# Kernel tuning notes

Measured on AMD Instinct MI355X. Metric: run time of the kernel, lower is better.

The kernel has to match this reference:

```python
import jax, jax.numpy as jnp
import numpy as np

VOCAB, EMBED, HIDDEN, PAD = 32000, 512, 1024, 3

def setup_inputs() -> dict:
    key = jax.random.key(0)
    ks = jax.random.split(key, 7)
    B, S = 16, 256
    input_ids = jax.random.randint(ks[0], (B, S), 0, VOCAB)
    hidden = jnp.zeros((B, HIDDEN), dtype=jnp.float32)
    sc = 0.02
    emb_table = jax.random.normal(ks[1], (VOCAB, EMBED), jnp.float32) * sc
    Wxh_w = jax.random.normal(ks[2], (HIDDEN, EMBED), jnp.float32) * sc
    Wxh_b = jax.random.normal(ks[3], (HIDDEN,), jnp.float32) * sc
    Whh_w = jax.random.normal(ks[4], (HIDDEN, HIDDEN), jnp.float32) * sc
    Who_w = jax.random.normal(ks[5], (VOCAB, HIDDEN), jnp.float32) * sc
    Who_b = jax.random.normal(ks[6], (VOCAB,), jnp.float32) * sc
    return {"input_ids": input_ids, "hidden": hidden, "emb_table": emb_table,
            "Wxh_w": Wxh_w, "Wxh_b": Wxh_b, "Whh_w": Whh_w,
            "Who_w": Who_w, "Who_b": Who_b}

def reference(input_ids, hidden, emb_table, Wxh_w, Wxh_b, Whh_w, Who_w, Who_b):
    # padding_idx: row PAD of the embedding is zero
    pad_mask = (jnp.arange(VOCAB) != PAD).astype(emb_table.dtype)
    table = emb_table * pad_mask[:, None]
    embeds = table[input_ids]                      # [B, S, E]
    # precompute input projection for all steps: [B, S, H]
    xproj = jnp.einsum('bse,he->bsh', embeds, Wxh_w) + Wxh_b

    def step(h, xp_t):                             # xp_t: [B, H]
        h_new = jnp.tanh(xp_t + h @ Whh_w.T)
        return h_new, h_new

    h_final, h_all = jax.lax.scan(step, hidden, jnp.swapaxes(xproj, 0, 1))
    # h_all: [S, B, H] -> logits [B, S, V]
    logits = jnp.einsum('sbh,vh->bsv', h_all, Who_w) + Who_b
    return (logits, h_final)
```

## Files before the change

### kernel.cpp

```cpp
#include <hip/hip_runtime.h>
#include <stdint.h>

#define NB 16
#define NS 256
#define NV 32000
#define NE 512
#define NH 1024
#define PAD_IDX 3

#define WS_XP    0L
#define WS_HCH   16777216L
#define WS_WHO   25198592L
#define WS_FLG   90734592L
#define WS_NEED  90800384L

typedef __attribute__((ext_vector_type(8))) short bf16x8;
typedef __attribute__((ext_vector_type(4))) float f32x4;
typedef __attribute__((ext_vector_type(4))) uint32_t u32x4;

__device__ __forceinline__ uint16_t f2bf(float f){
  union { float f; uint32_t u; } v; v.f = f;
  return (uint16_t)((v.u + 0x7fffu + ((v.u >> 16) & 1u)) >> 16);
}

__device__ __forceinline__ bf16x8 pack8(float4 a, float4 b){
  bf16x8 r;
  r[0]=(short)f2bf(a.x); r[1]=(short)f2bf(a.y); r[2]=(short)f2bf(a.z); r[3]=(short)f2bf(a.w);
  r[4]=(short)f2bf(b.x); r[5]=(short)f2bf(b.y); r[6]=(short)f2bf(b.z); r[7]=(short)f2bf(b.w);
  return r;
}

__device__ __forceinline__ u32x4 load_coh16(const void* p){
  u32x4 r;
  asm volatile("global_load_dwordx4 %0, %1, off sc0 sc1" : "=v"(r) : "v"(p) : "memory");
  return r;
}
__device__ __forceinline__ uint32_t load_coh4(const void* p){
  uint32_t r;
  asm volatile("global_load_dword %0, %1, off sc0 sc1" : "=v"(r) : "v"(p) : "memory");
  return r;
}
__device__ __forceinline__ void store_coh8(void* p, uint64_t v){
  asm volatile("global_store_dwordx2 %0, %1, off sc0 sc1" :: "v"(p), "v"(v) : "memory");
}
__device__ __forceinline__ void store_coh4(void* p, uint32_t v){
  asm volatile("global_store_dword %0, %1, off sc0 sc1" :: "v"(p), "v"(v) : "memory");
}
__device__ __forceinline__ void store_nt4(void* p, float v){
  asm volatile("global_store_dword %0, %1, off nt" :: "v"(p), "v"(v) : "memory");
}

__device__ __forceinline__ u32x4 umax4(u32x4 a, u32x4 b){
  u32x4 r;
  r[0] = a[0] > b[0] ? a[0] : b[0];
  r[1] = a[1] > b[1] ? a[1] : b[1];
  r[2] = a[2] > b[2] ? a[2] : b[2];
  r[3] = a[3] > b[3] ? a[3] : b[3];
  return r;
}

__device__ __forceinline__ float tanh_fast(float x){
  x = fminf(fmaxf(x, -10.f), 10.f);
  float t = __builtin_amdgcn_exp2f(x * 2.885390081777927f);
  return (t - 1.0f) * __builtin_amdgcn_rcpf(t + 1.0f);
}

__global__ void k_init(const float* __restrict__ hidden, uint16_t* __restrict__ hch,
                       uint32_t* __restrict__ flg){
  long idx = (long)blockIdx.x * 256 + threadIdx.x;
  ((u32x4*)(hch + (long)NB * NH))[idx] = (u32x4){~0u, ~0u, ~0u, ~0u};
  if (idx < NB * NH) hch[idx] = f2bf(hidden[idx]);
  if (idx < 512) flg[idx] = 0u;
}

__global__ void k_cvt(const float* __restrict__ src, uint32_t* __restrict__ dst){
  long idx = (long)blockIdx.x * 256 + threadIdx.x;
  const float4* p = (const float4*)src;
  float4 a = p[idx*2], b = p[idx*2+1];
  u32x4 d;
  d[0] = (uint32_t)f2bf(a.x) | ((uint32_t)f2bf(a.y) << 16);
  d[1] = (uint32_t)f2bf(a.z) | ((uint32_t)f2bf(a.w) << 16);
  d[2] = (uint32_t)f2bf(b.x) | ((uint32_t)f2bf(b.y) << 16);
  d[3] = (uint32_t)f2bf(b.z) | ((uint32_t)f2bf(b.w) << 16);
  ((u32x4*)dst)[idx] = d;
}

__global__ __launch_bounds__(256) void k_xproj(
    const int* __restrict__ ids, const float* __restrict__ tab,
    const float* __restrict__ wxh, const float* __restrict__ bxh,
    float* __restrict__ xp){
  int bid = blockIdx.x;
  int tm = bid & 63, tn = bid >> 6;
  int Mb = tm * 64, Nb = tn * 64;
  int tid = threadIdx.x;
  int w = tid >> 6, l = tid & 63;
  int lr = l & 15, lk = l >> 4;

  int m = Mb + w*16 + lr;
  int id = ids[m];
  const float* arow = tab + (long)id * NE;
  bool pad = (id == PAD_IDX);

  f32x4 acc[4];
  #pragma unroll
  for (int j = 0; j < 4; ++j) acc[j] = (f32x4){0.f,0.f,0.f,0.f};

  for (int k0 = 0; k0 < NE; k0 += 32){
    int k = k0 + lk*8;
    bf16x8 af = (bf16x8){0,0,0,0,0,0,0,0};
    if (!pad){
      float4 a = *(const float4*)(arow + k);
      float4 b = *(const float4*)(arow + k + 4);
      af = pack8(a, b);
    }
    #pragma unroll
    for (int j = 0; j < 4; ++j){
      const float* brow = wxh + (long)(Nb + j*16 + lr) * NE + k;
      float4 x = *(const float4*)brow;
      float4 y = *(const float4*)(brow + 4);
      bf16x8 bf_ = pack8(x, y);
      acc[j] = __builtin_amdgcn_mfma_f32_16x16x32_bf16(af, bf_, acc[j], 0, 0, 0);
    }
  }
  #pragma unroll
  for (int j = 0; j < 4; ++j){
    int n = Nb + j*16 + lr;
    float bias = bxh[n];
    #pragma unroll
    for (int r = 0; r < 4; ++r){
      int row = Mb + w*16 + lk*4 + r;
      xp[(long)row * NH + n] = acc[j][r] + bias;
    }
  }
}

__global__ __launch_bounds__(256, 2) void k_fused(
    const float* __restrict__ whh, const float* __restrict__ xp,
    uint16_t* __restrict__ hch, const uint16_t* __restrict__ whobf,
    const float* __restrict__ whob, uint32_t* __restrict__ allvis,
    uint32_t* __restrict__ fin, float* __restrict__ out,
    float* __restrict__ hfin){
  __shared__ __align__(16) char smem[17*1024];
  const int bid = blockIdx.x;
  const int tid = threadIdx.x;

  if (bid < 64){
    f32x4*    accbuf = (f32x4*)smem;
    uint16_t* hs2    = (uint16_t*)(smem + 6144);
    const int wv = tid >> 6;
    const int l  = tid & 63;
    const int j0 = bid * 16;
    const int lr = l & 15, lk = l >> 4;
    __builtin_amdgcn_s_setprio(2);

    bf16x8 bfrag[8];
    #pragma unroll
    for (int kk = 0; kk < 8; ++kk){
      const float* s0 = whh + (long)(j0 + lr) * NH + (wv*8 + kk)*32 + lk*8;
      float4 a = *(const float4*)s0;
      float4 b = *(const float4*)(s0 + 4);
      bfrag[kk] = pack8(a, b);
    }

    float xpreg[4];
    if (wv == 0){
      #pragma unroll
      for (int r = 0; r < 4; ++r)
        xpreg[r] = xp[((long)(lk*4 + r) * NS + 0) * NH + j0 + lr];
    }

    const char* hbase = (const char*)hch;
    for (int t = 0; t < NS; ++t){
      const char* hsrc = hbase + (long)t * NB * NH * 2 + lr * 2048 + wv * 512 + lk * 16;
      u32x4 hfrag[8];
      while (true){
        #pragma unroll
        for (int kk = 0; kk < 8; ++kk)
          hfrag[kk] = load_coh16(hsrc + kk * 64);
        asm volatile("s_waitcnt vmcnt(0)" ::: "memory");
        __builtin_amdgcn_sched_barrier(0);
        u32x4 m4 = hfrag[0];
        #pragma unroll
        for (int kk = 1; kk < 8; ++kk) m4 = umax4(m4, hfrag[kk]);
        uint32_t m01 = m4[0] > m4[1] ? m4[0] : m4[1];
        uint32_t m23 = m4[2] > m4[3] ? m4[2] : m4[3];
        uint32_t m = m01 > m23 ? m01 : m23;
        if (__all(m != 0xFFFFFFFFu)) break;
      }
      __builtin_amdgcn_sched_barrier(0);

      f32x4 a0 = (f32x4){0.f,0.f,0.f,0.f}, a1 = a0;
      #pragma unroll
      for (int kk = 0; kk < 8; kk += 2){
        a0 = __builtin_amdgcn_mfma_f32_16x16x32_bf16(*(const bf16x8*)&hfrag[kk  ], bfrag[kk  ], a0, 0, 0, 0);
        a1 = __builtin_amdgcn_mfma_f32_16x16x32_bf16(*(const bf16x8*)&hfrag[kk+1], bfrag[kk+1], a1, 0, 0, 0);
      }
      f32x4 acc = a0 + a1;

      if (wv != 0)
        accbuf[((t & 1)*3 + (wv-1))*64 + l] = acc;
      __syncthreads();

      if (wv == 0){
        if (bid == 0 && l == 0) store_coh4(allvis + t, 1u);
        f32x4 o0 = accbuf[((t & 1)*3 + 0)*64 + l];
        f32x4 o1 = accbuf[((t & 1)*3 + 1)*64 + l];
        f32x4 o2 = accbuf[((t & 1)*3 + 2)*64 + l];
        f32x4 osum = (acc + o0) + (o1 + o2);
        uint16_t* hb = hs2 + (t & 1)*256;
        #pragma unroll
        for (int r = 0; r < 4; ++r){
          int b = lk*4 + r;
          float hv = tanh_fast(xpreg[r] + osum[r]);
          hb[b*16 + lr] = f2bf(hv);
          if (t == NS-1) hfin[b*NH + j0 + lr] = hv;
        }
        asm volatile("s_waitcnt lgkmcnt(0)" ::: "memory");
        __builtin_amdgcn_sched_barrier(0);
        int rb = l >> 2, cc = l & 3;
        uint32_t w0 = *(const uint32_t*)&hb[rb*16 + cc*4];
        uint32_t w1 = *(const uint32_t*)&hb[rb*16 + cc*4 + 2];
        char* dst = (char*)hch + (long)(t+1) * NB * NH * 2 + rb * 2048 + j0*2 + cc*8;
        store_coh8(dst, ((uint64_t)w1 << 32) | (uint64_t)w0);
        if (t + 1 < NS){
          #pragma unroll
          for (int r = 0; r < 4; ++r)
            xpreg[r] = xp[((long)(lk*4 + r) * NS + (t+1)) * NH + j0 + lr];
        }
      }
    }
    if (wv == 0){
      asm volatile("s_waitcnt vmcnt(0)" ::: "memory");
      if (l == 0) store_coh4(fin + bid, 1u);
    }
    return;
  }

  uint16_t* As = (uint16_t*)smem;
  uint16_t* Bs = (uint16_t*)(smem + 8192);
  int tile = bid - 64;
  int tm = tile / 250;
  int tn = tile % 250;
  int Mb = tm * 128, Nb = tn * 128;
  int hs = tm * 8 + 8;

  if (hs < 256){
    while (true){
      uint32_t f = load_coh4(allvis + hs);
      asm volatile("s_waitcnt vmcnt(0)" ::: "memory");
      __builtin_amdgcn_sched_barrier(0);
      if (__syncthreads_count(f == 0u) == 0) break;
      __builtin_amdgcn_s_sleep(16);
    }
  } else {
    const uint32_t* gp = fin + (tid & 63);
    while (true){
      uint32_t f = load_coh4(gp);
      asm volatile("s_waitcnt vmcnt(0)" ::: "memory");
      __builtin_amdgcn_sched_barrier(0);
      if (__syncthreads_count(f == 0u) == 0) break;
      __builtin_amdgcn_s_sleep(16);
    }
  }

  int wv = tid >> 6, l = tid & 63;
  int wm = wv >> 1, wn = wv & 1;
  int lr = l & 15, lk = l >> 4;

  int r0 = tid >> 2, c0 = tid & 3;
  int r1 = r0 + 64;
  const uint16_t* pa0 = hch + (long)(Mb + r0 + 16) * NH + c0*8;
  const uint16_t* pa1 = hch + (long)(Mb + r1 + 16) * NH + c0*8;
  const uint16_t* pb0 = whobf + (long)(Nb + r0) * NH + c0*8;
  const uint16_t* pb1 = whobf + (long)(Nb + r1) * NH + c0*8;
  int da0 = r0*4 + (c0 ^ (r0 & 3));
  int da1 = r1*4 + (c0 ^ (r1 & 3));

  u32x4 ra0 = *(const u32x4*)pa0;
  u32x4 ra1 = *(const u32x4*)pa1;
  u32x4 rb0 = *(const u32x4*)pb0;
  u32x4 rb1 = *(const u32x4*)pb1;

  f32x4 acc[4][4];
  #pragma unroll
  for (int i = 0; i < 4; ++i)
    #pragma unroll
    for (int jj = 0; jj < 4; ++jj) acc[i][jj] = (f32x4){0.f,0.f,0.f,0.f};

  for (int kt = 0; kt < 32; ++kt){
    ((u32x4*)As)[da0] = ra0;
    ((u32x4*)As)[da1] = ra1;
    ((u32x4*)Bs)[da0] = rb0;
    ((u32x4*)Bs)[da1] = rb1;
    __syncthreads();
    if (kt != 31){
      int off = (kt + 1) * 32;
      ra0 = *(const u32x4*)(pa0 + off);
      ra1 = *(const u32x4*)(pa1 + off);
      rb0 = *(const u32x4*)(pb0 + off);
      rb1 = *(const u32x4*)(pb1 + off);
    }
    bf16x8 af[4], bg_[4];
    #pragma unroll
    for (int i = 0; i < 4; ++i){
      int ra = wm*64 + i*16 + lr;
      int rb = wn*64 + i*16 + lr;
      af[i]  = *(const bf16x8*)&((const u32x4*)As)[ra*4 + (lk ^ (ra & 3))];
      bg_[i] = *(const bf16x8*)&((const u32x4*)Bs)[rb*4 + (lk ^ (rb & 3))];
    }
    #pragma unroll
    for (int i = 0; i < 4; ++i)
      #pragma unroll
      for (int jj = 0; jj < 4; ++jj)
        acc[i][jj] = __builtin_amdgcn_mfma_f32_16x16x32_bf16(af[i], bg_[jj], acc[i][jj], 0, 0, 0);
    __syncthreads();
  }

  #pragma unroll
  for (int jj = 0; jj < 4; ++jj){
    int col = Nb + wn*64 + jj*16 + lr;
    float bias = whob[col];
    #pragma unroll
    for (int i = 0; i < 4; ++i){
      #pragma unroll
      for (int rr = 0; rr < 4; ++rr){
        int m = Mb + wm*64 + i*16 + lk*4 + rr;
        long orow = (long)((m & 15) * 256 + (m >> 4));
        store_nt4(&out[orow * NV + col], acc[i][jj][rr] + bias);
      }
    }
  }
}

extern "C" void kernel_launch(void* const* d_in, const int* in_sizes, int n_in,
                              void* d_out, int out_size, void* d_ws, size_t ws_size,
                              hipStream_t stream){
  (void)in_sizes; (void)n_in; (void)out_size;
  if (ws_size < (size_t)WS_NEED) return;

  const int*   ids    = (const int*)  d_in[0];
  const float* hidden = (const float*)d_in[1];
  const float* table  = (const float*)d_in[2];
  const float* wxh    = (const float*)d_in[3];
  const float* bxh    = (const float*)d_in[4];
  const float* whh    = (const float*)d_in[5];
  const float* who    = (const float*)d_in[6];
  const float* whob   = (const float*)d_in[7];

  char* ws = (char*)d_ws;
  float*    xp     = (float*)   (ws + WS_XP);
  uint16_t* hchain = (uint16_t*)(ws + WS_HCH);
  uint16_t* whobf  = (uint16_t*)(ws + WS_WHO);
  uint32_t* allvis = (uint32_t*)(ws + WS_FLG);
  uint32_t* fin    = allvis + 260;
  float* out    = (float*)d_out;
  float* hfinal = out + (long)NB * NS * NV;

  k_init <<<2048,  256, 0, stream>>>(hidden, hchain, allvis);
  k_cvt  <<<16000, 256, 0, stream>>>(who, (uint32_t*)whobf);
  k_xproj<<<1024,  256, 0, stream>>>(ids, table, wxh, bxh, xp);
  k_fused<<<8064,  256, 0, stream>>>(whh, xp, hchain, whobf, whob,
                                     allvis, fin, out, hfinal);
}
```

Measured before the change: 1.126 ms.

## Shrink recurrence to 16 blocks with full-K per wave via LDS-staged h

New measurement: 1.002 ms. 1.12x faster.

```diff
diff --git a/kernel.cpp b/kernel.cpp
--- a/kernel.cpp
+++ b/kernel.cpp
@@ -140,105 +140,98 @@
     const float* __restrict__ whob, uint32_t* __restrict__ allvis,
     uint32_t* __restrict__ fin, float* __restrict__ out,
     float* __restrict__ hfin){
-  __shared__ __align__(16) char smem[17*1024];
+  __shared__ __align__(16) char smem[35*1024];
   const int bid = blockIdx.x;
   const int tid = threadIdx.x;
 
-  if (bid < 64){
-    f32x4*    accbuf = (f32x4*)smem;
-    uint16_t* hs2    = (uint16_t*)(smem + 6144);
-    const int wv = tid >> 6;
-    const int l  = tid & 63;
-    const int j0 = bid * 16;
+  if (bid < 16){
+    uint16_t* hlds = (uint16_t*)smem;
+    uint16_t* hs2  = (uint16_t*)(smem + 32768);
+    const int wv = tid >> 6, l = tid & 63;
     const int lr = l & 15, lk = l >> 4;
+    const int base = bid*64 + wv*16;
     __builtin_amdgcn_s_setprio(2);
 
-    bf16x8 bfrag[8];
-    #pragma unroll
-    for (int kk = 0; kk < 8; ++kk){
-      const float* s0 = whh + (long)(j0 + lr) * NH + (wv*8 + kk)*32 + lk*8;
-      float4 a = *(const float4*)s0;
-      float4 b = *(const float4*)(s0 + 4);
-      bfrag[kk] = pack8(a, b);
+    bf16x8 wf[32];
+    #pragma unroll
+    for (int kk = 0; kk < 32; ++kk){
+      const float* s0 = whh + (long)(base + lr) * NH + kk*32 + lk*8;
+      wf[kk] = pack8(*(const float4*)s0, *(const float4*)(s0 + 4));
     }
 
     float xpreg[4];
-    if (wv == 0){
-      #pragma unroll
-      for (int r = 0; r < 4; ++r)
-        xpreg[r] = xp[((long)(lk*4 + r) * NS + 0) * NH + j0 + lr];
-    }
-
-    const char* hbase = (const char*)hch;
+    #pragma unroll
+    for (int r = 0; r < 4; ++r)
+      xpreg[r] = xp[((long)(lk*4 + r) * NS + 0) * NH + base + lr];
+
     for (int t = 0; t < NS; ++t){
-      const char* hsrc = hbase + (long)t * NB * NH * 2 + lr * 2048 + wv * 512 + lk * 16;
-      u32x4 hfrag[8];
-      while (true){
+      {
+        const char* ps = (const char*)hch + ((long)t * NB + (l >> 2)) * 2048
+                       + wv*512 + (l & 3)*128;
+        u32x4 hf[8];
+        while (true){
+          #pragma unroll
+          for (int j = 0; j < 8; ++j) hf[j] = load_coh16(ps + j*16);
+          asm volatile("s_waitcnt vmcnt(0)" ::: "memory");
+          __builtin_amdgcn_sched_barrier(0);
+          u32x4 m4 = hf[0];
+          #pragma unroll
+          for (int j = 1; j < 8; ++j) m4 = umax4(m4, hf[j]);
+          uint32_t m01 = m4[0] > m4[1] ? m4[0] : m4[1];
+          uint32_t m23 = m4[2] > m4[3] ? m4[2] : m4[3];
+          uint32_t m = m01 > m23 ? m01 : m23;
+          if (__all(m != 0xFFFFFFFFu)) break;
+        }
+        __builtin_amdgcn_sched_barrier(0);
+        int batch = l >> 2;
         #pragma unroll
-        for (int kk = 0; kk < 8; ++kk)
-          hfrag[kk] = load_coh16(hsrc + kk * 64);
-        asm volatile("s_waitcnt vmcnt(0)" ::: "memory");
-        __builtin_amdgcn_sched_barrier(0);
-        u32x4 m4 = hfrag[0];
-        #pragma unroll
-        for (int kk = 1; kk < 8; ++kk) m4 = umax4(m4, hfrag[kk]);
-        uint32_t m01 = m4[0] > m4[1] ? m4[0] : m4[1];
-        uint32_t m23 = m4[2] > m4[3] ? m4[2] : m4[3];
-        uint32_t m = m01 > m23 ? m01 : m23;
-        if (__all(m != 0xFFFFFFFFu)) break;
-      }
-      __builtin_amdgcn_sched_barrier(0);
+        for (int j = 0; j < 8; ++j){
+          int cib = wv*32 + (l & 3)*8 + j;
+          ((u32x4*)hlds)[batch*128 + (cib ^ (batch & 7))] = hf[j];
+        }
+      }
+      __syncthreads();
+      if (bid == 0 && tid == 0) store_coh4(allvis + t, 1u);
 
       f32x4 a0 = (f32x4){0.f,0.f,0.f,0.f}, a1 = a0;
       #pragma unroll
-      for (int kk = 0; kk < 8; kk += 2){
-        a0 = __builtin_amdgcn_mfma_f32_16x16x32_bf16(*(const bf16x8*)&hfrag[kk  ], bfrag[kk  ], a0, 0, 0, 0);
-        a1 = __builtin_amdgcn_mfma_f32_16x16x32_bf16(*(const bf16x8*)&hfrag[kk+1], bfrag[kk+1], a1, 0, 0, 0);
+      for (int kk = 0; kk < 32; kk += 2){
+        bf16x8 af0 = *(const bf16x8*)&((const u32x4*)hlds)[lr*128 + (( kk   *4 + lk) ^ (lr & 7))];
+        bf16x8 af1 = *(const bf16x8*)&((const u32x4*)hlds)[lr*128 + (((kk+1)*4 + lk) ^ (lr & 7))];
+        a0 = __builtin_amdgcn_mfma_f32_16x16x32_bf16(af0, wf[kk  ], a0, 0, 0, 0);
+        a1 = __builtin_amdgcn_mfma_f32_16x16x32_bf16(af1, wf[kk+1], a1, 0, 0, 0);
       }
       f32x4 acc = a0 + a1;
 
-      if (wv != 0)
-        accbuf[((t & 1)*3 + (wv-1))*64 + l] = acc;
+      #pragma unroll
+      for (int r = 0; r < 4; ++r){
+        float hv = tanh_fast(xpreg[r] + acc[r]);
+        hs2[(lk*4 + r)*64 + wv*16 + lr] = f2bf(hv);
+        if (t == NS-1) hfin[(long)(lk*4 + r) * NH + base + lr] = hv;
+      }
       __syncthreads();
 
-      if (wv == 0){
-        if (bid == 0 && l == 0) store_coh4(allvis + t, 1u);
-        f32x4 o0 = accbuf[((t & 1)*3 + 0)*64 + l];
-        f32x4 o1 = accbuf[((t & 1)*3 + 1)*64 + l];
-        f32x4 o2 = accbuf[((t & 1)*3 + 2)*64 + l];
-        f32x4 osum = (acc + o0) + (o1 + o2);
-        uint16_t* hb = hs2 + (t & 1)*256;
+      {
+        int row = tid >> 4, ch = tid & 15;
+        uint64_t v = *(const uint64_t*)&hs2[row*64 + ch*4];
+        char* dst = (char*)hch + ((long)(t+1) * NB + row) * 2048 + (bid*64 + ch*4)*2;
+        store_coh8(dst, v);
+      }
+      if (t + 1 < NS){
         #pragma unroll
-        for (int r = 0; r < 4; ++r){
-          int b = lk*4 + r;
-          float hv = tanh_fast(xpreg[r] + osum[r]);
-          hb[b*16 + lr] = f2bf(hv);
-          if (t == NS-1) hfin[b*NH + j0 + lr] = hv;
-        }
-        asm volatile("s_waitcnt lgkmcnt(0)" ::: "memory");
-        __builtin_amdgcn_sched_barrier(0);
-        int rb = l >> 2, cc = l & 3;
-        uint32_t w0 = *(const uint32_t*)&hb[rb*16 + cc*4];
-        uint32_t w1 = *(const uint32_t*)&hb[rb*16 + cc*4 + 2];
-        char* dst = (char*)hch + (long)(t+1) * NB * NH * 2 + rb * 2048 + j0*2 + cc*8;
-        store_coh8(dst, ((uint64_t)w1 << 32) | (uint64_t)w0);
-        if (t + 1 < NS){
-          #pragma unroll
-          for (int r = 0; r < 4; ++r)
-            xpreg[r] = xp[((long)(lk*4 + r) * NS + (t+1)) * NH + j0 + lr];
-        }
-      }
-    }
-    if (wv == 0){
-      asm volatile("s_waitcnt vmcnt(0)" ::: "memory");
-      if (l == 0) store_coh4(fin + bid, 1u);
-    }
+        for (int r = 0; r < 4; ++r)
+          xpreg[r] = xp[((long)(lk*4 + r) * NS + (t+1)) * NH + base + lr];
+      }
+    }
+    asm volatile("s_waitcnt vmcnt(0)" ::: "memory");
+    __syncthreads();
+    if (tid == 0) store_coh4(fin + bid, 1u);
     return;
   }
 
   uint16_t* As = (uint16_t*)smem;
   uint16_t* Bs = (uint16_t*)(smem + 8192);
-  int tile = bid - 64;
+  int tile = bid - 16;
   int tm = tile / 250;
   int tn = tile % 250;
   int Mb = tm * 128, Nb = tn * 128;
@@ -253,7 +246,7 @@
       __builtin_amdgcn_s_sleep(16);
     }
   } else {
-    const uint32_t* gp = fin + (tid & 63);
+    const uint32_t* gp = fin + (tid & 15);
     while (true){
       uint32_t f = load_coh4(gp);
       asm volatile("s_waitcnt vmcnt(0)" ::: "memory");
@@ -359,6 +352,6 @@
   k_init <<<2048,  256, 0, stream>>>(hidden, hchain, allvis);
   k_cvt  <<<16000, 256, 0, stream>>>(who, (uint32_t*)whobf);
   k_xproj<<<1024,  256, 0, stream>>>(ids, table, wxh, bxh, xp);
-  k_fused<<<8064,  256, 0, stream>>>(whh, xp, hchain, whobf, whob,
+  k_fused<<<8016,  256, 0, stream>>>(whh, xp, hchain, whobf, whob,
                                      allvis, fin, out, hfinal);
 }
```
